# Optimization experiments

Measured on AMD Instinct MI355X. Metric: run time of the kernel, lower is better.

Reference implementation:

```python
import jax, jax.numpy as jnp
import numpy as np

N_NODES = 50000
N_EDGES = 800000
HID = 64
N_GRAPHS = 512
RATIO = 0.5
EPS = 1e-12


def setup_inputs() -> dict:
    key = jax.random.key(0)
    k1, k2, k3, k4, k5 = jax.random.split(key, 5)
    emb = jax.random.normal(k1, (N_NODES, HID), dtype=jnp.float32)
    edge_index = jax.random.randint(k2, (2, N_EDGES), 0, N_NODES, dtype=jnp.int32)
    batch = jnp.sort(jax.random.randint(k3, (N_NODES,), 0, N_GRAPHS, dtype=jnp.int32))
    W1 = jax.random.normal(k4, (2 * HID, 4 * HID), dtype=jnp.float32) * 0.05
    b1 = jnp.zeros((4 * HID,), dtype=jnp.float32)
    W2 = jax.random.normal(k5, (4 * HID, 1), dtype=jnp.float32) * 0.05
    b2 = jnp.zeros((1,), dtype=jnp.float32)
    return {"emb": emb, "edge_index": edge_index, "batch": batch,
            "W1": W1, "b1": b1, "W2": W2, "b2": b2}


def _relabel(edge_index, keep):
    # node_mask[v] = 1 iff v appears as endpoint of any kept edge
    flat = edge_index.reshape(-1)                       # [2E]
    keep2 = jnp.concatenate([keep, keep]).astype(jnp.int32)
    flag = jnp.zeros((N_NODES,), jnp.int32).at[flat].max(keep2)
    node_mask = flag > 0
    # compact new ids (torch: node_idx[sub_nodes] = arange(len(sub_nodes)))
    node_idx = jnp.where(node_mask, jnp.cumsum(node_mask.astype(jnp.int32)) - 1, -1)
    ei_rel = jnp.where(keep[None, :], node_idx[edge_index], -1)  # [2,E], -1 on dropped edges
    return ei_rel


def reference(emb, edge_index, batch, W1, b1, W2, b2):
    row, col = edge_index[0], edge_index[1]
    # edge MLP scoring: cat([emb[row], emb[col]]) -> Linear -> ReLU -> Linear -> scalar
    edge_rep = jnp.concatenate([emb[row], emb[col]], axis=-1)          # [E, 2H]
    h = jax.nn.relu(edge_rep @ W1 + b1)                                # [E, 4H]
    edge_att = (h @ W2 + b2).reshape(-1)                               # [E]

    # --- sparse_topk (descending) over segments index = batch[row] ---
    index = batch[row]                                                 # [E] graph id per edge
    f = edge_att
    fmin, fmax = f.min(), f.max()
    norm = (f - fmin) / (fmax - fmin + EPS) - index.astype(f.dtype)    # (-1)**descending = -1
    perm = jnp.argsort(-norm)                                          # descending sort
    ones = jnp.ones((N_EDGES,), jnp.int32)
    deg = jax.ops.segment_sum(ones, index, num_segments=N_GRAPHS)      # edges per graph
    k = jnp.ceil(RATIO * deg.astype(jnp.float32)).astype(jnp.int32)
    cum = jnp.cumsum(deg)
    start = cum - deg                                                  # start index of each graph block
    seg_sorted = index[perm]
    pos = jnp.arange(N_EDGES, dtype=jnp.int32)
    mask_sorted = (pos - start[seg_sorted]) < k[seg_sorted]            # top-k within each block
    keep = jnp.zeros((N_EDGES,), bool).at[perm].set(mask_sorted)       # causal edges, original order

    causal_edge_weight = jnp.where(keep, edge_att, 0.0)
    spu_edge_weight = jnp.where(keep, 0.0, -edge_att)

    causal_ei_rel = _relabel(edge_index, keep)
    spu_ei_rel = _relabel(edge_index, ~keep)

    scores = jnp.stack([edge_att, causal_edge_weight, spu_edge_weight])  # [3, E]
    return scores, causal_ei_rel, spu_ei_rel
```

## Files before the change

### kernel.cpp

```cpp
#include <hip/hip_runtime.h>
#include <hip/hip_bf16.h>
#include <stdint.h>

#define N_NODES 50000
#define N_EDGES 800000
#define N_GRAPHS 512
#define NSUB 16
#define NBUCK (N_GRAPHS * NSUB)

__device__ __forceinline__ unsigned f2sort(float f) {
    unsigned u = __float_as_uint(f);
    return (u & 0x80000000u) ? ~u : (u | 0x80000000u);
}
__device__ __forceinline__ float sort2f(unsigned u) {
    return __uint_as_float((u & 0x80000000u) ? (u ^ 0x80000000u) : ~u);
}

__global__ __launch_bounds__(256) void k0_count(const int* __restrict__ ei,
                                                const int* __restrict__ batch,
                                                unsigned* __restrict__ subdeg,
                                                int* __restrict__ node_start) {
    __shared__ unsigned hist[NBUCK];
    const int tid = threadIdx.x;
    for (int i = tid; i < NBUCK; i += 256) hist[i] = 0;
    __syncthreads();
    const int e0 = blockIdx.x * 4096;
    #pragma unroll 4
    for (int j = 0; j < 16; ++j) {
        int e = e0 + j * 256 + tid;
        if (e < N_EDGES) {
            int r = ei[e], c = ei[N_EDGES + e];
            atomicAdd(&hist[batch[r] * NSUB + (c >> 12)], 1u);
        }
    }
    #pragma unroll 4
    for (int j = 0; j < 16; ++j) {
        int i = e0 + j * 256 + tid;
        if (i < N_NODES) {
            int b = batch[i];
            if (i == 0) { for (int g2 = 0; g2 <= b; ++g2) node_start[g2] = 0; }
            else { int bp = batch[i - 1]; for (int g2 = bp + 1; g2 <= b; ++g2) node_start[g2] = i; }
            if (i == N_NODES - 1) { for (int g2 = b + 1; g2 <= N_GRAPHS; ++g2) node_start[g2] = N_NODES; }
        }
    }
    __syncthreads();
    for (int i = tid; i < NBUCK; i += 256) {
        unsigned h = hist[i];
        if (h) atomicAdd(&subdeg[i], h);
    }
}

__global__ __launch_bounds__(1024) void k3_scan(const unsigned* __restrict__ subdeg,
                                                unsigned* __restrict__ substart,
                                                unsigned* __restrict__ deg,
                                                unsigned* __restrict__ start,
                                                unsigned* __restrict__ kkv) {
    __shared__ unsigned lds[1024];
    const int t = threadIdx.x;
    unsigned v[8], s = 0;
    #pragma unroll
    for (int j = 0; j < 8; ++j) { v[j] = subdeg[t * 8 + j]; s += v[j]; }
    lds[t] = s;
    for (int off = 1; off < 1024; off <<= 1) {
        __syncthreads();
        unsigned u = (t >= off) ? lds[t - off] : 0u;
        __syncthreads();
        lds[t] += u;
    }
    __syncthreads();
    unsigned run = lds[t] - s;
    #pragma unroll
    for (int j = 0; j < 8; ++j) { substart[t * 8 + j] = run; run += v[j]; }
    if (t == 1023) substart[NBUCK] = lds[1023];
    __syncthreads();
    if (t < N_GRAPHS) {
        unsigned st0 = substart[t * NSUB];
        unsigned d = substart[(t + 1) * NSUB] - st0;
        start[t] = st0;
        deg[t] = d;
        kkv[t] = (d + 1u) >> 1;
    }
}

__global__ __launch_bounds__(256) void k4a_scatter(const int* __restrict__ ei,
                                                   const int* __restrict__ batch,
                                                   const unsigned* __restrict__ substart,
                                                   unsigned* __restrict__ subcursor,
                                                   unsigned* __restrict__ rcbuck,
                                                   unsigned* __restrict__ ebuck,
                                                   unsigned* __restrict__ posOf) {
    int e = blockIdx.x * 256 + threadIdx.x;
    int r = ei[e], c = ei[N_EDGES + e];
    int b = batch[r] * NSUB + (c >> 12);
    unsigned rank = atomicAdd(&subcursor[b], 1u);
    unsigned pos = substart[b] + rank;
    rcbuck[pos] = (unsigned)r | ((unsigned)c << 16);
    ebuck[pos]  = (unsigned)e;
    posOf[e]    = pos;
}

__global__ __launch_bounds__(256) void k1_gemm(const float* __restrict__ emb,
                                               const float* __restrict__ W1,
                                               const float* __restrict__ b1,
                                               float* __restrict__ P,
                                               float* __restrict__ Q) {
    __shared__ float As[64][68];
    __shared__ float Bs[64][128];
    const int tid = threadIdx.x;
    const int v0  = blockIdx.x * 64;
    const int cy  = blockIdx.y;

    if (v0 + 64 <= N_NODES) {
        const float* srcA = emb + (size_t)v0 * 64;
        for (int idx = tid * 4; idx < 4096; idx += 1024) {
            float4 x = *(const float4*)(srcA + idx);
            int r = idx >> 6, k = idx & 63;
            As[k + 0][r] = x.x; As[k + 1][r] = x.y; As[k + 2][r] = x.z; As[k + 3][r] = x.w;
        }
    } else {
        for (int idx = tid * 4; idx < 4096; idx += 1024) {
            int r = idx >> 6, k = idx & 63;
            int v = v0 + r; if (v >= N_NODES) v = N_NODES - 1;
            float4 x = *(const float4*)(emb + (size_t)v * 64 + k);
            As[k + 0][r] = x.x; As[k + 1][r] = x.y; As[k + 2][r] = x.z; As[k + 3][r] = x.w;
        }
    }
    for (int idx = tid * 4; idx < 64 * 128; idx += 1024) {
        int k = idx >> 7, c = idx & 127;
        int jj = cy * 128 + c;
        const float* src = (jj < 256) ? (W1 + (size_t)k * 256 + jj)
                                      : (W1 + (size_t)(64 + k) * 256 + (jj - 256));
        *(float4*)&Bs[k][c] = *(const float4*)src;
    }
    __syncthreads();

    const int cgrp = tid & 31;
    const int rgrp = tid >> 5;
    float acc[8][4];
    #pragma unroll
    for (int r = 0; r < 8; ++r) { acc[r][0]=0.f; acc[r][1]=0.f; acc[r][2]=0.f; acc[r][3]=0.f; }

    #pragma unroll 8
    for (int k = 0; k < 64; ++k) {
        float4 b = *(const float4*)&Bs[k][cgrp * 4];
        const float4* ap = (const float4*)&As[k][rgrp * 8];
        float4 a01 = ap[0], a23 = ap[1];
        float av[8] = {a01.x, a01.y, a01.z, a01.w, a23.x, a23.y, a23.z, a23.w};
        #pragma unroll
        for (int r = 0; r < 8; ++r) {
            acc[r][0] = fmaf(av[r], b.x, acc[r][0]);
            acc[r][1] = fmaf(av[r], b.y, acc[r][1]);
            acc[r][2] = fmaf(av[r], b.z, acc[r][2]);
            acc[r][3] = fmaf(av[r], b.w, acc[r][3]);
        }
    }

    const int jj0 = cy * 128 + cgrp * 4;
    float4 badd = {0.f, 0.f, 0.f, 0.f};
    if (jj0 < 256) badd = *(const float4*)(b1 + jj0);
    #pragma unroll
    for (int r = 0; r < 8; ++r) {
        int v = v0 + rgrp * 8 + r;
        if (v < N_NODES) {
            float4 o = {acc[r][0] + badd.x, acc[r][1] + badd.y,
                        acc[r][2] + badd.z, acc[r][3] + badd.w};
            float* dst = (jj0 < 256) ? (P + (size_t)v * 256 + jj0)
                                     : (Q + (size_t)v * 256 + (jj0 - 256));
            *(float4*)dst = o;
        }
    }
}

__global__ __launch_bounds__(512) void k2_edge(const float* __restrict__ P,
                                               const float* __restrict__ Q,
                                               const unsigned* __restrict__ rcbuck,
                                               const unsigned* __restrict__ deg,
                                               const unsigned* __restrict__ start,
                                               const int* __restrict__ node_start,
                                               const float* __restrict__ W2,
                                               const float* __restrict__ b2,
                                               float* __restrict__ attb,
                                               unsigned* __restrict__ minmax,
                                               int ldsrows) {
    extern __shared__ float4 lds4[];
    const int g = blockIdx.x;
    const int n = (int)deg[g];
    if (n == 0) return;
    const int st = (int)start[g];
    const int n0 = node_start[g];
    const int nr = node_start[g + 1] - n0;
    const int ncap = nr < ldsrows ? nr : ldsrows;
    const int tid = threadIdx.x;

    const float4* Pg4 = (const float4*)(P + (size_t)n0 * 256);
    for (int u = tid; u < ncap * 64; u += 512) lds4[u] = Pg4[u];
    __syncthreads();

    const int lane = tid & 63;
    const int w = tid >> 6;
    const int j0 = lane * 4;
    const float4 w2v = *(const float4*)(W2 + j0);
    const float b2v = b2[0];
    float vmin = __builtin_inff(), vmax = -__builtin_inff();

    const int nquads = (n + 3) >> 2;
    for (int qi = w; qi < nquads; qi += 8) {
        const int i0 = st + qi * 4;
        int cnt = n - qi * 4; if (cnt > 4) cnt = 4;
        unsigned rc0 = rcbuck[i0];
        unsigned rc1 = (cnt > 1) ? rcbuck[i0 + 1] : (unsigned)n0;
        unsigned rc2 = (cnt > 2) ? rcbuck[i0 + 2] : (unsigned)n0;
        unsigned rc3 = (cnt > 3) ? rcbuck[i0 + 3] : (unsigned)n0;
        int r0 = rc0 & 0xFFFFu, c0 = rc0 >> 16;
        int r1 = rc1 & 0xFFFFu, c1 = rc1 >> 16;
        int r2 = rc2 & 0xFFFFu, c2 = rc2 >> 16;
        int r3 = rc3 & 0xFFFFu, c3 = rc3 >> 16;

        int rl0 = r0 - n0, rl1 = r1 - n0, rl2 = r2 - n0, rl3 = r3 - n0;
        float4 p0 = (rl0 < ncap) ? lds4[rl0 * 64 + lane] : *(const float4*)(P + (size_t)r0 * 256 + j0);
        float4 p1 = (rl1 < ncap) ? lds4[rl1 * 64 + lane] : *(const float4*)(P + (size_t)r1 * 256 + j0);
        float4 p2 = (rl2 < ncap) ? lds4[rl2 * 64 + lane] : *(const float4*)(P + (size_t)r2 * 256 + j0);
        float4 p3 = (rl3 < ncap) ? lds4[rl3 * 64 + lane] : *(const float4*)(P + (size_t)r3 * 256 + j0);
        float4 q0 = *(const float4*)(Q + (size_t)c0 * 256 + j0);
        float4 q1 = *(const float4*)(Q + (size_t)c1 * 256 + j0);
        float4 q2 = *(const float4*)(Q + (size_t)c2 * 256 + j0);
        float4 q3 = *(const float4*)(Q + (size_t)c3 * 256 + j0);

        float part0, part1, part2, part3;
        {
            float s0 = fmaxf(p0.x + q0.x, 0.f), s1 = fmaxf(p0.y + q0.y, 0.f);
            float s2 = fmaxf(p0.z + q0.z, 0.f), s3 = fmaxf(p0.w + q0.w, 0.f);
            part0 = fmaf(s3, w2v.w, fmaf(s2, w2v.z, fmaf(s1, w2v.y, s0 * w2v.x)));
        }
        {
            float s0 = fmaxf(p1.x + q1.x, 0.f), s1 = fmaxf(p1.y + q1.y, 0.f);
            float s2 = fmaxf(p1.z + q1.z, 0.f), s3 = fmaxf(p1.w + q1.w, 0.f);
            part1 = fmaf(s3, w2v.w, fmaf(s2, w2v.z, fmaf(s1, w2v.y, s0 * w2v.x)));
        }
        {
            float s0 = fmaxf(p2.x + q2.x, 0.f), s1 = fmaxf(p2.y + q2.y, 0.f);
            float s2 = fmaxf(p2.z + q2.z, 0.f), s3 = fmaxf(p2.w + q2.w, 0.f);
            part2 = fmaf(s3, w2v.w, fmaf(s2, w2v.z, fmaf(s1, w2v.y, s0 * w2v.x)));
        }
        {
            float s0 = fmaxf(p3.x + q3.x, 0.f), s1 = fmaxf(p3.y + q3.y, 0.f);
            float s2 = fmaxf(p3.z + q3.z, 0.f), s3 = fmaxf(p3.w + q3.w, 0.f);
            part3 = fmaf(s3, w2v.w, fmaf(s2, w2v.z, fmaf(s1, w2v.y, s0 * w2v.x)));
        }
        #pragma unroll
        for (int off = 32; off; off >>= 1) {
            part0 += __shfl_xor(part0, off, 64);
            part1 += __shfl_xor(part1, off, 64);
            part2 += __shfl_xor(part2, off, 64);
            part3 += __shfl_xor(part3, off, 64);
        }
        float a0 = part0 + b2v, a1 = part1 + b2v, a2 = part2 + b2v, a3 = part3 + b2v;
        if (lane == 0)                   attb[i0]     = a0;
        else if (lane == 1 && cnt > 1)   attb[i0 + 1] = a1;
        else if (lane == 2 && cnt > 2)   attb[i0 + 2] = a2;
        else if (lane == 3 && cnt > 3)   attb[i0 + 3] = a3;
        vmin = fminf(vmin, a0); vmax = fmaxf(vmax, a0);
        if (cnt > 1) { vmin = fminf(vmin, a1); vmax = fmaxf(vmax, a1); }
        if (cnt > 2) { vmin = fminf(vmin, a2); vmax = fmaxf(vmax, a2); }
        if (cnt > 3) { vmin = fminf(vmin, a3); vmax = fmaxf(vmax, a3); }
    }
    if (lane == 0) {
        atomicMin(&minmax[0], f2sort(vmin));
        atomicMax(&minmax[1], f2sort(vmax));
    }
}

__global__ __launch_bounds__(256) void k5_select(const unsigned* __restrict__ deg,
                                                 const unsigned* __restrict__ start,
                                                 const unsigned* __restrict__ kk,
                                                 const float* __restrict__ attb,
                                                 const unsigned* __restrict__ ebuck,
                                                 const unsigned* __restrict__ rcbuck,
                                                 const unsigned* __restrict__ minmax,
                                                 unsigned char* __restrict__ keepb,
                                                 unsigned char* __restrict__ flagC,
                                                 unsigned char* __restrict__ flagS) {
    __shared__ unsigned kbuf[4096];
    __shared__ unsigned hist[256];
    __shared__ unsigned sh_b, sh_excl, sh_cnt;
    const int g = blockIdx.x, t = threadIdx.x;
    int n = (int)deg[g]; if (n > 4096) n = 4096;
    if (n == 0) return;
    const unsigned st = start[g];
    const float fmin = sort2f(minmax[0]);
    const float fmax = sort2f(minmax[1]);
    const float denom = (fmax - fmin) + 1e-12f;
    const float gf = (float)g;
    for (int i = t; i < n; i += 256) {
        float a = attb[st + i];
        float nq = (a - fmin) / denom;
        float mq = nq - gf;
        kbuf[i] = ~f2sort(mq);
    }
    const unsigned K = kk[g];

    unsigned lo = 0, prefix = 0, meq = 0;
    for (int byte = 3; byte >= 0; --byte) {
        __syncthreads();
        hist[t] = 0;
        __syncthreads();
        const int shAbove = (byte + 1) * 8;
        for (int i = t; i < n; i += 256) {
            unsigned k = kbuf[i];
            bool ok = (byte == 3) || ((k >> shAbove) == (prefix >> shAbove));
            if (ok) atomicAdd(&hist[(k >> (byte * 8)) & 0xFFu], 1u);
        }
        __syncthreads();
        unsigned v = hist[t];
        for (int off = 1; off < 256; off <<= 1) {
            __syncthreads();
            unsigned u = (t >= off) ? hist[t - off] : 0u;
            __syncthreads();
            hist[t] += u;
        }
        __syncthreads();
        unsigned incl = hist[t], excl = incl - v;
        unsigned target = K - lo;
        if (excl < target && target <= incl) { sh_b = (unsigned)t; sh_excl = excl; sh_cnt = v; }
        __syncthreads();
        prefix |= sh_b << (byte * 8);
        lo += sh_excl;
        meq = sh_cnt;
    }
    const unsigned T32 = prefix;
    const unsigned tneed = K - lo;
    bool keepAllTies = (tneed == meq);

    unsigned E_t = 0xFFFFFFFFu;
    if (!keepAllTies) {
        unsigned elo = 0, eprefix = 0;
        for (int byte = 2; byte >= 0; --byte) {
            __syncthreads();
            hist[t] = 0;
            __syncthreads();
            const int shAbove = (byte + 1) * 8;
            for (int i = t; i < n; i += 256) {
                if (kbuf[i] == T32) {
                    unsigned e = ebuck[st + i];
                    bool ok = (byte == 2) || ((e >> shAbove) == (eprefix >> shAbove));
                    if (ok) atomicAdd(&hist[(e >> (byte * 8)) & 0xFFu], 1u);
                }
            }
            __syncthreads();
            unsigned v = hist[t];
            for (int off = 1; off < 256; off <<= 1) {
                __syncthreads();
                unsigned u = (t >= off) ? hist[t - off] : 0u;
                __syncthreads();
                hist[t] += u;
            }
            __syncthreads();
            unsigned incl = hist[t], excl = incl - v;
            unsigned target = tneed - elo;
            if (excl < target && target <= incl) { sh_b = (unsigned)t; sh_excl = excl; }
            __syncthreads();
            eprefix |= sh_b << (byte * 8);
            elo += sh_excl;
        }
        E_t = eprefix;
    }

    __syncthreads();
    for (int i = t; i < n; i += 256) {
        unsigned k = kbuf[i];
        bool kp = (k < T32) || (k == T32 && (keepAllTies || ebuck[st + i] <= E_t));
        keepb[st + i] = kp ? 1 : 0;
        unsigned rc = rcbuck[st + i];
        int r = (int)(rc & 0xFFFFu), c = (int)(rc >> 16);
        if (kp) { flagC[r] = 1; flagC[c] = 1; }
        else    { flagS[r] = 1; flagS[c] = 1; }
    }
}

__global__ __launch_bounds__(1024) void k7_nodescan(const unsigned char* __restrict__ flagC,
                                                    const unsigned char* __restrict__ flagS,
                                                    int* __restrict__ nidxC,
                                                    int* __restrict__ nidxS) {
    const unsigned char* fl = blockIdx.x ? flagS : flagC;
    int* nx = blockIdx.x ? nidxS : nidxC;
    __shared__ int lds[1024];
    const int t = threadIdx.x;
    const int CH = (N_NODES + 1023) / 1024;
    const int base = t * CH;
    int s = 0;
    for (int i = 0; i < CH; ++i) { int v = base + i; if (v < N_NODES) s += fl[v]; }
    lds[t] = s;
    for (int off = 1; off < 1024; off <<= 1) {
        __syncthreads();
        int v = (t >= off) ? lds[t - off] : 0;
        __syncthreads();
        lds[t] += v;
    }
    __syncthreads();
    int run = lds[t] - s;
    for (int i = 0; i < CH; ++i) {
        int v = base + i;
        if (v < N_NODES) {
            if (fl[v]) { nx[v] = run; run++; } else nx[v] = -1;
        }
    }
}

__global__ __launch_bounds__(256) void k8_out(const float* __restrict__ attb,
                                              const unsigned char* __restrict__ keepb,
                                              const unsigned* __restrict__ posOf,
                                              const int* __restrict__ ei,
                                              const int* __restrict__ nidxC,
                                              const int* __restrict__ nidxS,
                                              float* __restrict__ out) {
    int e = blockIdx.x * 256 + threadIdx.x;
    unsigned pos = posOf[e];
    float a = attb[pos];
    int kp = keepb[pos];
    int r = ei[e], c = ei[N_EDGES + e];
    out[e]               = a;
    out[N_EDGES + e]     = kp ? a : 0.f;
    out[2 * N_EDGES + e] = kp ? 0.f : -a;
    if (kp) {
        out[3 * N_EDGES + e] = (float)nidxC[r];
        out[4 * N_EDGES + e] = (float)nidxC[c];
        out[5 * N_EDGES + e] = -1.f;
        out[6 * N_EDGES + e] = -1.f;
    } else {
        out[3 * N_EDGES + e] = -1.f;
        out[4 * N_EDGES + e] = -1.f;
        out[5 * N_EDGES + e] = (float)nidxS[r];
        out[6 * N_EDGES + e] = (float)nidxS[c];
    }
}

extern "C" void kernel_launch(void* const* d_in, const int* in_sizes, int n_in,
                              void* d_out, int out_size, void* d_ws, size_t ws_size,
                              hipStream_t stream) {
    const float* emb   = (const float*)d_in[0];
    const int*   ei    = (const int*)d_in[1];
    const int*   batch = (const int*)d_in[2];
    const float* W1    = (const float*)d_in[3];
    const float* b1    = (const float*)d_in[4];
    const float* W2    = (const float*)d_in[5];
    const float* b2    = (const float*)d_in[6];
    float* out = (float*)d_out;

    char* ws = (char*)d_ws;
    size_t off = 0;
    auto alloc = [&](size_t bytes) -> void* {
        off = (off + 255) & ~(size_t)255;
        void* p = ws + off;
        off += bytes;
        return p;
    };

    float* P              = (float*)alloc((size_t)N_NODES * 256 * 4);
    float* Q              = (float*)alloc((size_t)N_NODES * 256 * 4);
    float* attb           = (float*)alloc((size_t)N_EDGES * 4);
    unsigned* rcbuck      = (unsigned*)alloc(((size_t)N_EDGES + 8) * 4);
    unsigned* ebuck       = (unsigned*)alloc(((size_t)N_EDGES + 8) * 4);
    unsigned* posOf       = (unsigned*)alloc((size_t)N_EDGES * 4);
    unsigned char* keepb  = (unsigned char*)alloc(N_EDGES);
    unsigned char* flags2 = (unsigned char*)alloc((size_t)2 * N_NODES);
    unsigned char* flagC  = flags2;
    unsigned char* flagS  = flags2 + N_NODES;
    int* nidxC            = (int*)alloc((size_t)N_NODES * 4);
    int* nidxS            = (int*)alloc((size_t)N_NODES * 4);
    unsigned* meta        = (unsigned*)alloc((2 * NBUCK + 3 * 512 + 2) * 4);
    unsigned* subdeg      = meta;
    unsigned* subcursor   = meta + NBUCK;
    unsigned* deg         = meta + 2 * NBUCK;
    unsigned* start       = meta + 2 * NBUCK + 512;
    unsigned* kk          = meta + 2 * NBUCK + 1024;
    unsigned* minmax      = meta + 2 * NBUCK + 1536;
    unsigned* substart    = (unsigned*)alloc((NBUCK + 1) * 4);
    int* node_start       = (int*)alloc(513 * 4);

    const int EB = (N_EDGES + 255) / 256;
    const int SB = (N_EDGES + 4095) / 4096;

    hipMemsetAsync(meta, 0, (2 * NBUCK + 3 * 512 + 2) * 4, stream);
    hipMemsetAsync(minmax, 0xFF, 4, stream);
    hipMemsetAsync(flags2, 0, (size_t)2 * N_NODES, stream);

    int ldsrows = 78;
    if (hipFuncSetAttribute((const void*)k2_edge,
                            hipFuncAttributeMaxDynamicSharedMemorySize,
                            78 * 1024) != hipSuccess) {
        ldsrows = 56;
    }
    const size_t shbytes = (size_t)ldsrows * 1024;

    k0_count<<<SB, 256, 0, stream>>>(ei, batch, subdeg, node_start);
    k3_scan<<<1, 1024, 0, stream>>>(subdeg, substart, deg, start, kk);
    k4a_scatter<<<EB, 256, 0, stream>>>(ei, batch, substart, subcursor, rcbuck, ebuck, posOf);

    dim3 g1((N_NODES + 63) / 64, 4);
    k1_gemm<<<g1, 256, 0, stream>>>(emb, W1, b1, P, Q);

    k2_edge<<<N_GRAPHS, 512, shbytes, stream>>>(P, Q, rcbuck, deg, start,
                                                node_start, W2, b2, attb, minmax, ldsrows);

    k5_select<<<N_GRAPHS, 256, 0, stream>>>(deg, start, kk, attb, ebuck, rcbuck,
                                            minmax, keepb, flagC, flagS);
    k7_nodescan<<<2, 1024, 0, stream>>>(flagC, flagS, nidxC, nidxS);
    k8_out<<<EB, 256, 0, stream>>>(attb, keepb, posOf, ei, nidxC, nidxS, out);
}
```

Baseline: 406.3 us.

## Write edge scores in original order and process eight edges per wave

```diff
diff --git a/kernel.cpp b/kernel.cpp
--- a/kernel.cpp
+++ b/kernel.cpp
@@ -87,8 +87,7 @@
                                                    const unsigned* __restrict__ substart,
                                                    unsigned* __restrict__ subcursor,
                                                    unsigned* __restrict__ rcbuck,
-                                                   unsigned* __restrict__ ebuck,
-                                                   unsigned* __restrict__ posOf) {
+                                                   unsigned* __restrict__ ebuck) {
     int e = blockIdx.x * 256 + threadIdx.x;
     int r = ei[e], c = ei[N_EDGES + e];
     int b = batch[r] * NSUB + (c >> 12);
@@ -96,7 +95,6 @@
     unsigned pos = substart[b] + rank;
     rcbuck[pos] = (unsigned)r | ((unsigned)c << 16);
     ebuck[pos]  = (unsigned)e;
-    posOf[e]    = pos;
 }
 
 __global__ __launch_bounds__(256) void k1_gemm(const float* __restrict__ emb,
@@ -171,17 +169,18 @@
     }
 }
 
-__global__ __launch_bounds__(512) void k2_edge(const float* __restrict__ P,
-                                               const float* __restrict__ Q,
-                                               const unsigned* __restrict__ rcbuck,
-                                               const unsigned* __restrict__ deg,
-                                               const unsigned* __restrict__ start,
-                                               const int* __restrict__ node_start,
-                                               const float* __restrict__ W2,
-                                               const float* __restrict__ b2,
-                                               float* __restrict__ attb,
-                                               unsigned* __restrict__ minmax,
-                                               int ldsrows) {
+__global__ __launch_bounds__(512, 4) void k2_edge(const float* __restrict__ P,
+                                                  const float* __restrict__ Q,
+                                                  const unsigned* __restrict__ rcbuck,
+                                                  const unsigned* __restrict__ ebuck,
+                                                  const unsigned* __restrict__ deg,
+                                                  const unsigned* __restrict__ start,
+                                                  const int* __restrict__ node_start,
+                                                  const float* __restrict__ W2,
+                                                  const float* __restrict__ b2,
+                                                  float* __restrict__ att,
+                                                  unsigned* __restrict__ minmax,
+                                                  int ldsrows) {
     extern __shared__ float4 lds4[];
     const int g = blockIdx.x;
     const int n = (int)deg[g];
@@ -203,66 +202,54 @@
     const float b2v = b2[0];
     float vmin = __builtin_inff(), vmax = -__builtin_inff();
 
-    const int nquads = (n + 3) >> 2;
-    for (int qi = w; qi < nquads; qi += 8) {
-        const int i0 = st + qi * 4;
-        int cnt = n - qi * 4; if (cnt > 4) cnt = 4;
-        unsigned rc0 = rcbuck[i0];
-        unsigned rc1 = (cnt > 1) ? rcbuck[i0 + 1] : (unsigned)n0;
-        unsigned rc2 = (cnt > 2) ? rcbuck[i0 + 2] : (unsigned)n0;
-        unsigned rc3 = (cnt > 3) ? rcbuck[i0 + 3] : (unsigned)n0;
-        int r0 = rc0 & 0xFFFFu, c0 = rc0 >> 16;
-        int r1 = rc1 & 0xFFFFu, c1 = rc1 >> 16;
-        int r2 = rc2 & 0xFFFFu, c2 = rc2 >> 16;
-        int r3 = rc3 & 0xFFFFu, c3 = rc3 >> 16;
-
-        int rl0 = r0 - n0, rl1 = r1 - n0, rl2 = r2 - n0, rl3 = r3 - n0;
-        float4 p0 = (rl0 < ncap) ? lds4[rl0 * 64 + lane] : *(const float4*)(P + (size_t)r0 * 256 + j0);
-        float4 p1 = (rl1 < ncap) ? lds4[rl1 * 64 + lane] : *(const float4*)(P + (size_t)r1 * 256 + j0);
-        float4 p2 = (rl2 < ncap) ? lds4[rl2 * 64 + lane] : *(const float4*)(P + (size_t)r2 * 256 + j0);
-        float4 p3 = (rl3 < ncap) ? lds4[rl3 * 64 + lane] : *(const float4*)(P + (size_t)r3 * 256 + j0);
-        float4 q0 = *(const float4*)(Q + (size_t)c0 * 256 + j0);
-        float4 q1 = *(const float4*)(Q + (size_t)c1 * 256 + j0);
-        float4 q2 = *(const float4*)(Q + (size_t)c2 * 256 + j0);
-        float4 q3 = *(const float4*)(Q + (size_t)c3 * 256 + j0);
-
-        float part0, part1, part2, part3;
-        {
-            float s0 = fmaxf(p0.x + q0.x, 0.f), s1 = fmaxf(p0.y + q0.y, 0.f);
-            float s2 = fmaxf(p0.z + q0.z, 0.f), s3 = fmaxf(p0.w + q0.w, 0.f);
-            part0 = fmaf(s3, w2v.w, fmaf(s2, w2v.z, fmaf(s1, w2v.y, s0 * w2v.x)));
-        }
-        {
-            float s0 = fmaxf(p1.x + q1.x, 0.f), s1 = fmaxf(p1.y + q1.y, 0.f);
-            float s2 = fmaxf(p1.z + q1.z, 0.f), s3 = fmaxf(p1.w + q1.w, 0.f);
-            part1 = fmaf(s3, w2v.w, fmaf(s2, w2v.z, fmaf(s1, w2v.y, s0 * w2v.x)));
-        }
-        {
-            float s0 = fmaxf(p2.x + q2.x, 0.f), s1 = fmaxf(p2.y + q2.y, 0.f);
-            float s2 = fmaxf(p2.z + q2.z, 0.f), s3 = fmaxf(p2.w + q2.w, 0.f);
-            part2 = fmaf(s3, w2v.w, fmaf(s2, w2v.z, fmaf(s1, w2v.y, s0 * w2v.x)));
-        }
-        {
-            float s0 = fmaxf(p3.x + q3.x, 0.f), s1 = fmaxf(p3.y + q3.y, 0.f);
-            float s2 = fmaxf(p3.z + q3.z, 0.f), s3 = fmaxf(p3.w + q3.w, 0.f);
-            part3 = fmaf(s3, w2v.w, fmaf(s2, w2v.z, fmaf(s1, w2v.y, s0 * w2v.x)));
+    const int noct = (n + 7) >> 3;
+    for (int oi = w; oi < noct; oi += 8) {
+        const int i0 = st + oi * 8;
+        int cnt = n - oi * 8; if (cnt > 8) cnt = 8;
+        uint4 rcA = *(const uint4*)(rcbuck + i0);
+        uint4 rcB = *(const uint4*)(rcbuck + i0 + 4);
+        uint4 evA = *(const uint4*)(ebuck + i0);
+        uint4 evB = *(const uint4*)(ebuck + i0 + 4);
+        unsigned rc[8] = {rcA.x, rcA.y, rcA.z, rcA.w, rcB.x, rcB.y, rcB.z, rcB.w};
+        unsigned ev[8] = {evA.x, evA.y, evA.z, evA.w, evB.x, evB.y, evB.z, evB.w};
+
+        float4 p[8], q[8];
+        #pragma unroll
+        for (int j = 0; j < 8; ++j) {
+            int r = (int)(rc[j] & 0xFFFFu);
+            int c = (int)(rc[j] >> 16);
+            int rl = r - n0;
+            q[j] = *(const float4*)(Q + (size_t)c * 256 + j0);
+            p[j] = (rl < ncap && rl >= 0) ? lds4[rl * 64 + lane]
+                                          : *(const float4*)(P + (size_t)r * 256 + j0);
+        }
+
+        float part[8];
+        #pragma unroll
+        for (int j = 0; j < 8; ++j) {
+            float s0 = fmaxf(p[j].x + q[j].x, 0.f);
+            float s1 = fmaxf(p[j].y + q[j].y, 0.f);
+            float s2 = fmaxf(p[j].z + q[j].z, 0.f);
+            float s3 = fmaxf(p[j].w + q[j].w, 0.f);
+            part[j] = fmaf(s3, w2v.w, fmaf(s2, w2v.z, fmaf(s1, w2v.y, s0 * w2v.x)));
         }
         #pragma unroll
         for (int off = 32; off; off >>= 1) {
-            part0 += __shfl_xor(part0, off, 64);
-            part1 += __shfl_xor(part1, off, 64);
-            part2 += __shfl_xor(part2, off, 64);
-            part3 += __shfl_xor(part3, off, 64);
-        }
-        float a0 = part0 + b2v, a1 = part1 + b2v, a2 = part2 + b2v, a3 = part3 + b2v;
-        if (lane == 0)                   attb[i0]     = a0;
-        else if (lane == 1 && cnt > 1)   attb[i0 + 1] = a1;
-        else if (lane == 2 && cnt > 2)   attb[i0 + 2] = a2;
-        else if (lane == 3 && cnt > 3)   attb[i0 + 3] = a3;
-        vmin = fminf(vmin, a0); vmax = fmaxf(vmax, a0);
-        if (cnt > 1) { vmin = fminf(vmin, a1); vmax = fmaxf(vmax, a1); }
-        if (cnt > 2) { vmin = fminf(vmin, a2); vmax = fmaxf(vmax, a2); }
-        if (cnt > 3) { vmin = fminf(vmin, a3); vmax = fmaxf(vmax, a3); }
+            #pragma unroll
+            for (int j = 0; j < 8; ++j) part[j] += __shfl_xor(part[j], off, 64);
+        }
+        float av = part[0]; unsigned ew = ev[0];
+        #pragma unroll
+        for (int j = 1; j < 8; ++j) if (lane == j) { av = part[j]; ew = ev[j]; }
+        if (lane < cnt) att[ew] = av + b2v;
+
+        #pragma unroll
+        for (int j = 0; j < 8; ++j) {
+            if (j < cnt) {
+                float a = part[j] + b2v;
+                vmin = fminf(vmin, a); vmax = fmaxf(vmax, a);
+            }
+        }
     }
     if (lane == 0) {
         atomicMin(&minmax[0], f2sort(vmin));
@@ -273,11 +260,11 @@
 __global__ __launch_bounds__(256) void k5_select(const unsigned* __restrict__ deg,
                                                  const unsigned* __restrict__ start,
                                                  const unsigned* __restrict__ kk,
-                                                 const float* __restrict__ attb,
+                                                 const float* __restrict__ att,
                                                  const unsigned* __restrict__ ebuck,
                                                  const unsigned* __restrict__ rcbuck,
                                                  const unsigned* __restrict__ minmax,
-                                                 unsigned char* __restrict__ keepb,
+                                                 unsigned char* __restrict__ keep,
                                                  unsigned char* __restrict__ flagC,
                                                  unsigned char* __restrict__ flagS) {
     __shared__ unsigned kbuf[4096];
@@ -292,7 +279,7 @@
     const float denom = (fmax - fmin) + 1e-12f;
     const float gf = (float)g;
     for (int i = t; i < n; i += 256) {
-        float a = attb[st + i];
+        float a = att[ebuck[st + i]];
         float nq = (a - fmin) / denom;
         float mq = nq - gf;
         kbuf[i] = ~f2sort(mq);
@@ -368,8 +355,9 @@
     __syncthreads();
     for (int i = t; i < n; i += 256) {
         unsigned k = kbuf[i];
-        bool kp = (k < T32) || (k == T32 && (keepAllTies || ebuck[st + i] <= E_t));
-        keepb[st + i] = kp ? 1 : 0;
+        unsigned e = ebuck[st + i];
+        bool kp = (k < T32) || (k == T32 && (keepAllTies || e <= E_t));
+        keep[e] = kp ? 1 : 0;
         unsigned rc = rcbuck[st + i];
         int r = (int)(rc & 0xFFFFu), c = (int)(rc >> 16);
         if (kp) { flagC[r] = 1; flagC[c] = 1; }
@@ -406,17 +394,15 @@
     }
 }
 
-__global__ __launch_bounds__(256) void k8_out(const float* __restrict__ attb,
-                                              const unsigned char* __restrict__ keepb,
-                                              const unsigned* __restrict__ posOf,
+__global__ __launch_bounds__(256) void k8_out(const float* __restrict__ att,
+                                              const unsigned char* __restrict__ keep,
                                               const int* __restrict__ ei,
                                               const int* __restrict__ nidxC,
                                               const int* __restrict__ nidxS,
                                               float* __restrict__ out) {
     int e = blockIdx.x * 256 + threadIdx.x;
-    unsigned pos = posOf[e];
-    float a = attb[pos];
-    int kp = keepb[pos];
+    float a = att[e];
+    int kp = keep[e];
     int r = ei[e], c = ei[N_EDGES + e];
     out[e]               = a;
     out[N_EDGES + e]     = kp ? a : 0.f;
@@ -457,11 +443,10 @@
 
     float* P              = (float*)alloc((size_t)N_NODES * 256 * 4);
     float* Q              = (float*)alloc((size_t)N_NODES * 256 * 4);
-    float* attb           = (float*)alloc((size_t)N_EDGES * 4);
+    float* att            = (float*)alloc((size_t)N_EDGES * 4);
     unsigned* rcbuck      = (unsigned*)alloc(((size_t)N_EDGES + 8) * 4);
     unsigned* ebuck       = (unsigned*)alloc(((size_t)N_EDGES + 8) * 4);
-    unsigned* posOf       = (unsigned*)alloc((size_t)N_EDGES * 4);
-    unsigned char* keepb  = (unsigned char*)alloc(N_EDGES);
+    unsigned char* keep   = (unsigned char*)alloc(N_EDGES);
     unsigned char* flags2 = (unsigned char*)alloc((size_t)2 * N_NODES);
     unsigned char* flagC  = flags2;
     unsigned char* flagS  = flags2 + N_NODES;
@@ -494,16 +479,16 @@
 
     k0_count<<<SB, 256, 0, stream>>>(ei, batch, subdeg, node_start);
     k3_scan<<<1, 1024, 0, stream>>>(subdeg, substart, deg, start, kk);
-    k4a_scatter<<<EB, 256, 0, stream>>>(ei, batch, substart, subcursor, rcbuck, ebuck, posOf);
+    k4a_scatter<<<EB, 256, 0, stream>>>(ei, batch, substart, subcursor, rcbuck, ebuck);
 
     dim3 g1((N_NODES + 63) / 64, 4);
     k1_gemm<<<g1, 256, 0, stream>>>(emb, W1, b1, P, Q);
 
-    k2_edge<<<N_GRAPHS, 512, shbytes, stream>>>(P, Q, rcbuck, deg, start,
-                                                node_start, W2, b2, attb, minmax, ldsrows);
-
-    k5_select<<<N_GRAPHS, 256, 0, stream>>>(deg, start, kk, attb, ebuck, rcbuck,
-                                            minmax, keepb, flagC, flagS);
+    k2_edge<<<N_GRAPHS, 512, shbytes, stream>>>(P, Q, rcbuck, ebuck, deg, start,
+                                                node_start, W2, b2, att, minmax, ldsrows);
+
+    k5_select<<<N_GRAPHS, 256, 0, stream>>>(deg, start, kk, att, ebuck, rcbuck,
+                                            minmax, keep, flagC, flagS);
     k7_nodescan<<<2, 1024, 0, stream>>>(flagC, flagS, nidxC, nidxS);
-    k8_out<<<EB, 256, 0, stream>>>(attb, keepb, posOf, ei, nidxC, nidxS, out);
-}
+    k8_out<<<EB, 256, 0, stream>>>(att, keep, ei, nidxC, nidxS, out);
+}
```

Result: no change. 407.6 us (+0.3%).
